# Performance work log

Hardware: AMD Instinct MI355X
Metric: run time of the kernel (lower is better)

The kernel has to match this reference:

```python
import jax, jax.numpy as jnp
import numpy as np

PATCH = 96
STRIDE = PATCH // 2  # 48


def setup_inputs() -> dict:
    key = jax.random.key(0)
    kx = jax.random.fold_in(key, 0)
    x = jax.random.uniform(kx, (8, 4, 1056, 1056), dtype=jnp.float32)
    mu_pristine = jnp.zeros((36,), dtype=jnp.float32)
    cov_pristine = jnp.eye(36, dtype=jnp.float32)
    return {"x": x, "mu_pristine": mu_pristine, "cov_pristine": cov_pristine}


def _extract_patches(x):
    # x: [B, C, H, W] -> overlapping patches [B, C, N, P, P], stride = P//2
    B, C, H, W = x.shape
    nH = (H - PATCH) // STRIDE + 1
    nW = (W - PATCH) // STRIDE + 1
    idx_h = np.arange(nH)[:, None] * STRIDE + np.arange(PATCH)[None, :]  # [nH, P]
    idx_w = np.arange(nW)[:, None] * STRIDE + np.arange(PATCH)[None, :]  # [nW, P]
    p = x[:, :, idx_h, :]            # [B, C, nH, P, W]
    p = p[:, :, :, :, idx_w]         # [B, C, nH, P, nW, P]
    p = p.transpose(0, 1, 2, 4, 3, 5)  # [B, C, nH, nW, P, P]
    return p.reshape(B, C, nH * nW, PATCH, PATCH)


def reference(x, mu_pristine, cov_pristine):
    patches = _extract_patches(x)  # [B, C, N, P, P]
    mu = patches.mean(axis=(-2, -1))                    # [B, C, N]
    var = patches.var(axis=(-2, -1), ddof=1)            # unbiased, matches torch.var
    gx = jnp.diff(patches, axis=-1)                     # [B, C, N, P, P-1]
    gy = jnp.diff(patches, axis=-2)                     # [B, C, N, P-1, P]
    grad_mag = jnp.sqrt((gx * gx).mean(axis=(-2, -1)) + (gy * gy).mean(axis=(-2, -1)))
    # torch concatenates [mu, var, grad_mag] along channel dim per patch, then means over patches
    feats = jnp.concatenate([mu, var, grad_mag], axis=1).mean(axis=-1)  # [B, 3C]
    d = feats.shape[1]
    mu0 = mu_pristine[:d]
    cov_inv = jnp.linalg.inv(cov_pristine[:d, :d])
    diff = feats - mu0[None, :]
    dist = jnp.sqrt(((diff @ cov_inv) * diff).sum(axis=1))  # Mahalanobis distance [B]
    return dist.mean()
```

## Files before the change

kernel.cpp:

```cpp
#include <hip/hip_runtime.h>
#include <math.h>

#define PATCH 96
#define STRIDE 48
#define NH 21
#define NW 21
#define NP (NH * NW)
#define BATCH 8
#define CHAN 4
#define NBC (BATCH * CHAN)
#define IMG_H 1056
#define IMG_W 1056
#define NHB 44
#define NCHUNK 22
#define NSTAT 6
#define NPIX 9216.0f
#define NGRAD 9120.0f
#define SLAB (NHB * NCHUNK * NSTAT)

__global__ __launch_bounds__(320) void band_stats_kernel(
    const float* __restrict__ x, float* __restrict__ pf, int* __restrict__ cnt) {
  __shared__ float acc[NCHUNK * NSTAT];

  const int t = threadIdx.x;
  const int bc = blockIdx.x / NHB;
  const int hb = blockIdx.x - bc * NHB;
  if (blockIdx.x == 0 && t == 0) cnt[0] = 0;

  const bool active = t < 264;
  const int tc = active ? t : 263;
  const int noff = (tc == 263) ? 3 : 4;

  const float* rowbase = x + (size_t)bc * (IMG_H * IMG_W)
                           + (size_t)(hb * 24) * IMG_W
                           + (size_t)(4 * tc);

  float s1 = 0.f, s2 = 0.f, gxi = 0.f, gxb = 0.f, gyi = 0.f, gyb = 0.f;
  const bool bnd_is_gxb = ((tc % 12) == 11);

#define SUMS_GX(A, nxt)                                                  \
  do {                                                                   \
    s1 += (A).x + (A).y + (A).z + (A).w;                                 \
    s2 += (A).x * (A).x + (A).y * (A).y + (A).z * (A).z + (A).w * (A).w; \
    float d1 = (A).y - (A).x, d2 = (A).z - (A).y, d3 = (A).w - (A).z;    \
    float d4 = (nxt) - (A).w;                                            \
    gxi += d1 * d1 + d2 * d2 + d3 * d3;                                  \
    float bd = d4 * d4;                                                  \
    if (bnd_is_gxb) gxb += bd; else gxi += bd;                           \
  } while (0)

  float4 prev;
  {
    const float4 A = *(const float4*)rowbase;
    const float nxt = rowbase[noff];
    SUMS_GX(A, nxt);
    prev = A;
  }
#pragma unroll 4
  for (int r = 1; r < 24; ++r) {
    const float4 A = *(const float4*)(rowbase + (size_t)r * IMG_W);
    const float nxt = rowbase[(size_t)r * IMG_W + noff];
    SUMS_GX(A, nxt);
    const float e0 = A.x - prev.x, e1 = A.y - prev.y,
                e2 = A.z - prev.z, e3 = A.w - prev.w;
    gyi += e0 * e0 + e1 * e1 + e2 * e2 + e3 * e3;
    prev = A;
  }
  if (hb != NHB - 1) {
    const float4 A = *(const float4*)(rowbase + (size_t)24 * IMG_W);
    const float e0 = A.x - prev.x, e1 = A.y - prev.y,
                e2 = A.z - prev.z, e3 = A.w - prev.w;
    gyb = e0 * e0 + e1 * e1 + e2 * e2 + e3 * e3;
  }
#undef SUMS_GX

  for (int i = t; i < NCHUNK * NSTAT; i += 320) acc[i] = 0.f;
  __syncthreads();
  if (active) {
    const int chunk = tc / 12;
    atomicAdd(&acc[chunk * NSTAT + 0], s1);
    atomicAdd(&acc[chunk * NSTAT + 1], s2);
    atomicAdd(&acc[chunk * NSTAT + 2], gxi);
    atomicAdd(&acc[chunk * NSTAT + 3], gxb);
    atomicAdd(&acc[chunk * NSTAT + 4], gyi);
    atomicAdd(&acc[chunk * NSTAT + 5], gyb);
  }
  __syncthreads();
  float* dst = pf + (size_t)(bc * NHB + hb) * (NCHUNK * NSTAT);
  for (int i = t; i < NCHUNK * NSTAT; i += 320) dst[i] = acc[i];
}

__global__ __launch_bounds__(512) void patch_finalize_kernel(
    const float* __restrict__ pf, float* __restrict__ featsG,
    int* __restrict__ cnt, const float* __restrict__ mu0_full,
    const float* __restrict__ cov_full, float* __restrict__ out) {
  __shared__ float S[SLAB];
  __shared__ float wsum[8][3];
  __shared__ double inv_s[12][12];
  __shared__ float fin_s[96 + BATCH];
  __shared__ int ticket_s;

  const int bc = blockIdx.x;
  const int t = threadIdx.x;
  const float* src = pf + (size_t)bc * SLAB;
  for (int i = t; i < SLAB; i += 512) S[i] = src[i];
  __syncthreads();

  float fmu = 0.f, fvar = 0.f, fg = 0.f;
  if (t < NP) {
    const int ph = t / NW, pw = t - ph * NW;
    const int h0 = 2 * ph;
#define AT(h, c, s) S[((h) * NCHUNK + (c)) * NSTAT + (s)]
    float S1 = 0.f, S2 = 0.f, Gx = 0.f, Gy = 0.f;
#pragma unroll
    for (int hh = 0; hh < 4; ++hh) {
      const int h = h0 + hh;
      S1 += AT(h, pw, 0) + AT(h, pw + 1, 0);
      S2 += AT(h, pw, 1) + AT(h, pw + 1, 1);
      Gx += AT(h, pw, 2) + AT(h, pw, 3) + AT(h, pw + 1, 2);
      Gy += AT(h, pw, 4) + AT(h, pw + 1, 4);
    }
#pragma unroll
    for (int hh = 0; hh < 3; ++hh) {
      const int h = h0 + hh;
      Gy += AT(h, pw, 5) + AT(h, pw + 1, 5);
    }
#undef AT
    fmu = S1 / NPIX;
    fvar = (S2 - S1 * S1 / NPIX) / (NPIX - 1.f);
    fg = sqrtf((Gx + Gy) / NGRAD);
  }
#pragma unroll
  for (int off = 32; off > 0; off >>= 1) {
    fmu += __shfl_xor(fmu, off);
    fvar += __shfl_xor(fvar, off);
    fg += __shfl_xor(fg, off);
  }
  const int wave = t >> 6;
  if ((t & 63) == 0) { wsum[wave][0] = fmu; wsum[wave][1] = fvar; wsum[wave][2] = fg; }
  __syncthreads();
  if (t == 0) {
    float m = 0.f, v = 0.f, g = 0.f;
#pragma unroll
    for (int w = 0; w < 8; ++w) { m += wsum[w][0]; v += wsum[w][1]; g += wsum[w][2]; }
    const int b = bc / CHAN, c = bc - b * CHAN;
    featsG[b * 12 + 0 + c] = m / (float)NP;
    featsG[b * 12 + 4 + c] = v / (float)NP;
    featsG[b * 12 + 8 + c] = g / (float)NP;
    __threadfence();
    ticket_s = atomicAdd(cnt, 1);
  }
  __syncthreads();
  if (ticket_s != NBC - 1) return;

  __threadfence();
  if (t < 96)
    fin_s[t] = __hip_atomic_load(&featsG[t], __ATOMIC_RELAXED,
                                 __HIP_MEMORY_SCOPE_AGENT);
  __syncthreads();

  if (t < 64) {
    double M[12];
#pragma unroll
    for (int r = 0; r < 12; ++r) {
      double v = 0.0;
      if (t < 12) v = (double)cov_full[r * 36 + t];
      else if (t < 24) v = (t - 12 == r) ? 1.0 : 0.0;
      M[r] = v;
    }
#pragma unroll
    for (int k = 0; k < 12; ++k) {
      const double piv = __shfl(M[k], k);
      const double ip = 1.0 / piv;
      M[k] *= ip;
#pragma unroll
      for (int r = 0; r < 12; ++r) {
        if (r == k) continue;
        const double f = __shfl(M[r], k);
        M[r] -= f * M[k];
      }
    }
    if (t >= 12 && t < 24) {
      const int j = t - 12;
#pragma unroll
      for (int r = 0; r < 12; ++r) inv_s[r][j] = M[r];
    }
  }
  __syncthreads();

  if (t < BATCH) {
    double acc = 0.0;
    double d[12];
#pragma unroll
    for (int i = 0; i < 12; ++i)
      d[i] = (double)fin_s[t * 12 + i] - (double)mu0_full[i];
#pragma unroll
    for (int i = 0; i < 12; ++i) {
      double row = 0.0;
#pragma unroll
      for (int j = 0; j < 12; ++j) row += inv_s[i][j] * d[j];
      acc += d[i] * row;
    }
    fin_s[96 + t] = (float)sqrt(acc);
  }
  __syncthreads();
  if (t == 0) {
    float m = 0.f;
#pragma unroll
    for (int b = 0; b < BATCH; ++b) m += fin_s[96 + b];
    out[0] = m / (float)BATCH;
  }
}

extern "C" void kernel_launch(void* const* d_in, const int* in_sizes, int n_in,
                              void* d_out, int out_size, void* d_ws, size_t ws_size,
                              hipStream_t stream) {
  const float* x   = (const float*)d_in[0];
  const float* mu0 = (const float*)d_in[1];
  const float* cov = (const float*)d_in[2];
  float* out = (float*)d_out;
  float* pf     = (float*)d_ws;
  float* featsG = pf + (size_t)NBC * SLAB;
  int* cnt      = (int*)(featsG + 96);

  band_stats_kernel<<<NBC * NHB, 320, 0, stream>>>(x, pf, cnt);
  patch_finalize_kernel<<<NBC, 512, 0, stream>>>(pf, featsG, cnt, mu0, cov, out);
}
```

Measured before the change: 227.6 us.

## Double-buffer row bands into LDS with async global_load_lds staging

Each block's band rows are now staged five at a time into a double-buffered LDS tile using the AMD global-to-LDS direct load builtin. The next row group is prefetched while the current one is processed, so each thread's float4 and neighbour reads come from LDS instead of separate global loads. The goal is to overlap memory latency with compute and remove the redundant global read of the neighbour element. The cost is about 42 KB of LDS per block, which limits occupancy, plus extra barriers. It also depends on the compiler inserting the right wait counts before each barrier.

Result: slower. 238.2 us (+4.7%).

```diff
diff --git a/kernel.cpp b/kernel.cpp
--- a/kernel.cpp
+++ b/kernel.cpp
@@ -11,15 +11,25 @@
 #define NBC (BATCH * CHAN)
 #define IMG_H 1056
 #define IMG_W 1056
+#define ROWF 1056
 #define NHB 44
 #define NCHUNK 22
 #define NSTAT 6
 #define NPIX 9216.0f
 #define NGRAD 9120.0f
 #define SLAB (NHB * NCHUNK * NSTAT)
+#define RB 5
+
+typedef __attribute__((address_space(3))) unsigned int lds_uint;
+typedef __attribute__((address_space(1))) const unsigned int glb_uint;
+
+__device__ __forceinline__ void stage16(const float* g, float* l) {
+  __builtin_amdgcn_global_load_lds((glb_uint*)g, (lds_uint*)l, 16, 0, 0);
+}
 
 __global__ __launch_bounds__(320) void band_stats_kernel(
     const float* __restrict__ x, float* __restrict__ pf, int* __restrict__ cnt) {
+  __shared__ float L[2][RB * ROWF];
   __shared__ float acc[NCHUNK * NSTAT];
 
   const int t = threadIdx.x;
@@ -31,12 +41,26 @@
   const int tc = active ? t : 263;
   const int noff = (tc == 263) ? 3 : 4;
 
-  const float* rowbase = x + (size_t)bc * (IMG_H * IMG_W)
-                           + (size_t)(hb * 24) * IMG_W
-                           + (size_t)(4 * tc);
+  const float* base = x + (size_t)bc * (IMG_H * IMG_W);
+  const int row0 = hb * 24;
+  const int wbase = (t >> 6) << 8;
+
+#define STAGE(bt, bufi)                                                   \
+  do {                                                                    \
+    if (active) {                                                         \
+      _Pragma("unroll")                                                   \
+      for (int rr = 0; rr < RB; ++rr) {                                   \
+        int grow = row0 + (bt) * RB + rr;                                 \
+        if (grow > IMG_H - 1) grow = IMG_H - 1;                           \
+        stage16(base + (size_t)grow * ROWF + 4 * tc,                      \
+                &L[bufi][rr * ROWF + wbase]);                             \
+      }                                                                   \
+    }                                                                     \
+  } while (0)
 
   float s1 = 0.f, s2 = 0.f, gxi = 0.f, gxb = 0.f, gyi = 0.f, gyb = 0.f;
   const bool bnd_is_gxb = ((tc % 12) == 11);
+  float4 prev{0.f, 0.f, 0.f, 0.f};
 
 #define SUMS_GX(A, nxt)                                                  \
   do {                                                                   \
@@ -49,30 +73,32 @@
     if (bnd_is_gxb) gxb += bd; else gxi += bd;                           \
   } while (0)
 
-  float4 prev;
-  {
-    const float4 A = *(const float4*)rowbase;
-    const float nxt = rowbase[noff];
-    SUMS_GX(A, nxt);
-    prev = A;
-  }
-#pragma unroll 4
-  for (int r = 1; r < 24; ++r) {
-    const float4 A = *(const float4*)(rowbase + (size_t)r * IMG_W);
-    const float nxt = rowbase[(size_t)r * IMG_W + noff];
-    SUMS_GX(A, nxt);
-    const float e0 = A.x - prev.x, e1 = A.y - prev.y,
-                e2 = A.z - prev.z, e3 = A.w - prev.w;
-    gyi += e0 * e0 + e1 * e1 + e2 * e2 + e3 * e3;
-    prev = A;
-  }
-  if (hb != NHB - 1) {
-    const float4 A = *(const float4*)(rowbase + (size_t)24 * IMG_W);
-    const float e0 = A.x - prev.x, e1 = A.y - prev.y,
-                e2 = A.z - prev.z, e3 = A.w - prev.w;
-    gyb = e0 * e0 + e1 * e1 + e2 * e2 + e3 * e3;
+  STAGE(0, 0);
+  __syncthreads();
+#pragma unroll
+  for (int bt = 0; bt < 5; ++bt) {
+    if (bt < 4) STAGE(bt + 1, (bt + 1) & 1);
+    const float* Lb = &L[bt & 1][0];
+#pragma unroll
+    for (int rr = 0; rr < RB; ++rr) {
+      const int ri = bt * RB + rr;
+      const float4 A = *(const float4*)&Lb[rr * ROWF + 4 * tc];
+      if (ri < 24) {
+        const float nxt = Lb[rr * ROWF + 4 * tc + noff];
+        SUMS_GX(A, nxt);
+      }
+      if (ri > 0) {
+        const float e0 = A.x - prev.x, e1 = A.y - prev.y,
+                    e2 = A.z - prev.z, e3 = A.w - prev.w;
+        const float sq = e0 * e0 + e1 * e1 + e2 * e2 + e3 * e3;
+        if (ri < 24) gyi += sq; else gyb += sq;
+      }
+      prev = A;
+    }
+    __syncthreads();
   }
 #undef SUMS_GX
+#undef STAGE
 
   for (int i = t; i < NCHUNK * NSTAT; i += 320) acc[i] = 0.f;
   __syncthreads();
```

## Stage row loads into LDS asynchronously with a four-row software prefetch pipeline

Applied to the files above, without the earlier changes.

Replaces the per-row direct float4 global loads in the band statistics kernel with `global_load_lds` transfers into a five-slot per-wave LDS ring. Loads are issued four rows ahead and throttled by explicit `s_waitcnt vmcnt` counts, and the loop is fully unrolled. The goal is to keep more memory requests in flight and hide global latency in a kernel whose effective bandwidth is far below peak. It relies on exact hand-counted vmcnt values and on the LDS load builtin's per-lane layout. On the last band the extra boundary row is redirected to a valid row.

New measurement: 240.8 us. +5.8%, slower.

```diff
diff --git a/kernel.cpp b/kernel.cpp
--- a/kernel.cpp
+++ b/kernel.cpp
@@ -11,15 +11,26 @@
 #define NBC (BATCH * CHAN)
 #define IMG_H 1056
 #define IMG_W 1056
+#define ROWF 1056
 #define NHB 44
 #define NCHUNK 22
 #define NSTAT 6
 #define NPIX 9216.0f
 #define NGRAD 9120.0f
 #define SLAB (NHB * NCHUNK * NSTAT)
+#define NR 5
+#define PF 4
+
+typedef __attribute__((address_space(3))) unsigned int lds_uint;
+typedef __attribute__((address_space(1))) const unsigned int glb_uint;
+
+__device__ __forceinline__ void stage16(const float* g, float* l) {
+  __builtin_amdgcn_global_load_lds((glb_uint*)g, (lds_uint*)l, 16, 0, 0);
+}
 
 __global__ __launch_bounds__(320) void band_stats_kernel(
-    const float* __restrict__ x, float* __restrict__ pf, int* __restrict__ cnt) {
+    const float* __restrict__ x, float* __restrict__ pfo, int* __restrict__ cnt) {
+  __shared__ float L[5 * NR * 256];
   __shared__ float acc[NCHUNK * NSTAT];
 
   const int t = threadIdx.x;
@@ -30,49 +41,70 @@
   const bool active = t < 264;
   const int tc = active ? t : 263;
   const int noff = (tc == 263) ? 3 : 4;
-
-  const float* rowbase = x + (size_t)bc * (IMG_H * IMG_W)
-                           + (size_t)(hb * 24) * IMG_W
-                           + (size_t)(4 * tc);
+  const int lane = t & 63;
+  const int wave = t >> 6;
+
+  const float* base = x + (size_t)bc * (IMG_H * IMG_W);
+  const int row0 = hb * 24;
+  float* Lw = &L[wave * (NR * 256)];
 
   float s1 = 0.f, s2 = 0.f, gxi = 0.f, gxb = 0.f, gyi = 0.f, gyb = 0.f;
   const bool bnd_is_gxb = ((tc % 12) == 11);
-
-#define SUMS_GX(A, nxt)                                                  \
+  float4 prev{0.f, 0.f, 0.f, 0.f};
+  float nxt[NR];
+
+#define GROWN(r) (((r) == 24 && hb == NHB - 1) ? (row0 + 23) : (row0 + (r)))
+
+#define ISSUE(r)                                                         \
+  do {                                                                   \
+    const float* g_ = base + (size_t)GROWN(r) * ROWF + 4 * tc;           \
+    stage16(g_, Lw + ((r) % NR) * 256);                                  \
+    nxt[(r) % NR] = g_[noff];                                            \
+  } while (0)
+
+#define SUMS_GX(A, nx)                                                   \
   do {                                                                   \
     s1 += (A).x + (A).y + (A).z + (A).w;                                 \
     s2 += (A).x * (A).x + (A).y * (A).y + (A).z * (A).z + (A).w * (A).w; \
     float d1 = (A).y - (A).x, d2 = (A).z - (A).y, d3 = (A).w - (A).z;    \
-    float d4 = (nxt) - (A).w;                                            \
+    float d4 = (nx) - (A).w;                                             \
     gxi += d1 * d1 + d2 * d2 + d3 * d3;                                  \
     float bd = d4 * d4;                                                  \
     if (bnd_is_gxb) gxb += bd; else gxi += bd;                           \
   } while (0)
 
-  float4 prev;
-  {
-    const float4 A = *(const float4*)rowbase;
-    const float nxt = rowbase[noff];
-    SUMS_GX(A, nxt);
-    prev = A;
-  }
-#pragma unroll 4
-  for (int r = 1; r < 24; ++r) {
-    const float4 A = *(const float4*)(rowbase + (size_t)r * IMG_W);
-    const float nxt = rowbase[(size_t)r * IMG_W + noff];
-    SUMS_GX(A, nxt);
-    const float e0 = A.x - prev.x, e1 = A.y - prev.y,
-                e2 = A.z - prev.z, e3 = A.w - prev.w;
-    gyi += e0 * e0 + e1 * e1 + e2 * e2 + e3 * e3;
-    prev = A;
-  }
-  if (hb != NHB - 1) {
-    const float4 A = *(const float4*)(rowbase + (size_t)24 * IMG_W);
-    const float e0 = A.x - prev.x, e1 = A.y - prev.y,
-                e2 = A.z - prev.z, e3 = A.w - prev.w;
-    gyb = e0 * e0 + e1 * e1 + e2 * e2 + e3 * e3;
-  }
+#define CONSUME(r)                                                       \
+  do {                                                                   \
+    const float4 A = *(const float4*)(Lw + ((r) % NR) * 256 + lane * 4); \
+    if ((r) < 24) SUMS_GX(A, nxt[(r) % NR]);                             \
+    if ((r) > 0) {                                                       \
+      const float e0 = A.x - prev.x, e1 = A.y - prev.y,                  \
+                  e2 = A.z - prev.z, e3 = A.w - prev.w;                  \
+      const float sq = e0 * e0 + e1 * e1 + e2 * e2 + e3 * e3;            \
+      if ((r) < 24) gyi += sq; else gyb += sq;                           \
+    }                                                                    \
+    prev = A;                                                            \
+  } while (0)
+
+#define STEP(r, w)                                                       \
+  do {                                                                   \
+    if ((r) + PF <= 24) ISSUE((r) + PF);                                 \
+    asm volatile("s_waitcnt vmcnt(" #w ")" ::: "memory");                \
+    CONSUME(r);                                                          \
+  } while (0)
+
+  ISSUE(0); ISSUE(1); ISSUE(2); ISSUE(3);
+  STEP(0, 8);  STEP(1, 8);  STEP(2, 8);  STEP(3, 8);  STEP(4, 8);
+  STEP(5, 8);  STEP(6, 8);  STEP(7, 8);  STEP(8, 8);  STEP(9, 8);
+  STEP(10, 8); STEP(11, 8); STEP(12, 8); STEP(13, 8); STEP(14, 8);
+  STEP(15, 8); STEP(16, 8); STEP(17, 8); STEP(18, 8); STEP(19, 8);
+  STEP(20, 8);
+  STEP(21, 6); STEP(22, 4); STEP(23, 2); STEP(24, 0);
+#undef STEP
+#undef CONSUME
 #undef SUMS_GX
+#undef ISSUE
+#undef GROWN
 
   for (int i = t; i < NCHUNK * NSTAT; i += 320) acc[i] = 0.f;
   __syncthreads();
@@ -86,7 +118,7 @@
     atomicAdd(&acc[chunk * NSTAT + 5], gyb);
   }
   __syncthreads();
-  float* dst = pf + (size_t)(bc * NHB + hb) * (NCHUNK * NSTAT);
+  float* dst = pfo + (size_t)(bc * NHB + hb) * (NCHUNK * NSTAT);
   for (int i = t; i < NCHUNK * NSTAT; i += 320) dst[i] = acc[i];
 }
 
```

## Drop per-block LDS atomics; write per-column partials and reduce in finalize

Applied to the files above, without the earlier changes.

The stats kernel no longer pads threads to 320 per band or accumulates into shared memory with atomics. Instead it launches exactly one thread per 4-column strip and writes six per-thread partial sums straight to global memory in a column-major layout. The finalize kernel now performs the 12-wide chunk reduction while loading its shared slab. This removes shared-memory atomics, block syncs and idle threads from the bandwidth-bound stage. In exchange it writes a much larger partial buffer and makes the single-wave-per-image finalize kernel do extra strided global reads.

After: 230.9 us. Within noise of the previous version (+1.4%).

```diff
diff --git a/kernel.cpp b/kernel.cpp
--- a/kernel.cpp
+++ b/kernel.cpp
@@ -11,42 +11,40 @@
 #define NBC (BATCH * CHAN)
 #define IMG_H 1056
 #define IMG_W 1056
+#define ROWF 1056
 #define NHB 44
+#define NQ 264
 #define NCHUNK 22
 #define NSTAT 6
 #define NPIX 9216.0f
 #define NGRAD 9120.0f
-#define SLAB (NHB * NCHUNK * NSTAT)
-
-__global__ __launch_bounds__(320) void band_stats_kernel(
+#define CSLAB (NHB * NCHUNK * NSTAT)
+#define QSLAB (NHB * NSTAT * NQ)
+#define NTHREADS (NBC * NHB * NQ)
+
+__global__ __launch_bounds__(256) void strip_stats_kernel(
     const float* __restrict__ x, float* __restrict__ pf, int* __restrict__ cnt) {
-  __shared__ float acc[NCHUNK * NSTAT];
-
-  const int t = threadIdx.x;
-  const int bc = blockIdx.x / NHB;
-  const int hb = blockIdx.x - bc * NHB;
-  if (blockIdx.x == 0 && t == 0) cnt[0] = 0;
-
-  const bool active = t < 264;
-  const int tc = active ? t : 263;
-  const int noff = (tc == 263) ? 3 : 4;
-
-  const float* rowbase = x + (size_t)bc * (IMG_H * IMG_W)
-                           + (size_t)(hb * 24) * IMG_W
-                           + (size_t)(4 * tc);
+  const int g = blockIdx.x * 256 + threadIdx.x;
+  if (g == 0) cnt[0] = 0;
+
+  const int qcol = g % NQ;
+  const int bh = g / NQ;
+  const int hb = bh % NHB;
+  const int noff = (qcol == NQ - 1) ? 3 : 4;
+
+  const float* rowbase = x + (size_t)(bh / NHB) * (IMG_H * IMG_W)
+                           + (size_t)(hb * 24) * ROWF + 4 * qcol;
 
   float s1 = 0.f, s2 = 0.f, gxi = 0.f, gxb = 0.f, gyi = 0.f, gyb = 0.f;
-  const bool bnd_is_gxb = ((tc % 12) == 11);
-
-#define SUMS_GX(A, nxt)                                                  \
+
+#define SUMS_GX(A, nx)                                                   \
   do {                                                                   \
     s1 += (A).x + (A).y + (A).z + (A).w;                                 \
     s2 += (A).x * (A).x + (A).y * (A).y + (A).z * (A).z + (A).w * (A).w; \
     float d1 = (A).y - (A).x, d2 = (A).z - (A).y, d3 = (A).w - (A).z;    \
-    float d4 = (nxt) - (A).w;                                            \
+    float d4 = (nx) - (A).w;                                             \
     gxi += d1 * d1 + d2 * d2 + d3 * d3;                                  \
-    float bd = d4 * d4;                                                  \
-    if (bnd_is_gxb) gxb += bd; else gxi += bd;                           \
+    gxb += d4 * d4;                                                      \
   } while (0)
 
   float4 prev;
@@ -56,45 +54,39 @@
     SUMS_GX(A, nxt);
     prev = A;
   }
-#pragma unroll 4
+#pragma unroll
   for (int r = 1; r < 24; ++r) {
-    const float4 A = *(const float4*)(rowbase + (size_t)r * IMG_W);
-    const float nxt = rowbase[(size_t)r * IMG_W + noff];
+    const float4 A = *(const float4*)(rowbase + (size_t)r * ROWF);
+    const float nxt = rowbase[(size_t)r * ROWF + noff];
     SUMS_GX(A, nxt);
     const float e0 = A.x - prev.x, e1 = A.y - prev.y,
                 e2 = A.z - prev.z, e3 = A.w - prev.w;
     gyi += e0 * e0 + e1 * e1 + e2 * e2 + e3 * e3;
     prev = A;
   }
-  if (hb != NHB - 1) {
-    const float4 A = *(const float4*)(rowbase + (size_t)24 * IMG_W);
+  {
+    const int r24 = (hb == NHB - 1) ? 23 : 24;
+    const float4 A = *(const float4*)(rowbase + (size_t)r24 * ROWF);
     const float e0 = A.x - prev.x, e1 = A.y - prev.y,
                 e2 = A.z - prev.z, e3 = A.w - prev.w;
     gyb = e0 * e0 + e1 * e1 + e2 * e2 + e3 * e3;
   }
 #undef SUMS_GX
 
-  for (int i = t; i < NCHUNK * NSTAT; i += 320) acc[i] = 0.f;
-  __syncthreads();
-  if (active) {
-    const int chunk = tc / 12;
-    atomicAdd(&acc[chunk * NSTAT + 0], s1);
-    atomicAdd(&acc[chunk * NSTAT + 1], s2);
-    atomicAdd(&acc[chunk * NSTAT + 2], gxi);
-    atomicAdd(&acc[chunk * NSTAT + 3], gxb);
-    atomicAdd(&acc[chunk * NSTAT + 4], gyi);
-    atomicAdd(&acc[chunk * NSTAT + 5], gyb);
-  }
-  __syncthreads();
-  float* dst = pf + (size_t)(bc * NHB + hb) * (NCHUNK * NSTAT);
-  for (int i = t; i < NCHUNK * NSTAT; i += 320) dst[i] = acc[i];
+  float* dst = pf + (size_t)bh * (NSTAT * NQ) + qcol;
+  dst[0 * NQ] = s1;
+  dst[1 * NQ] = s2;
+  dst[2 * NQ] = gxi;
+  dst[3 * NQ] = gxb;
+  dst[4 * NQ] = gyi;
+  dst[5 * NQ] = gyb;
 }
 
 __global__ __launch_bounds__(512) void patch_finalize_kernel(
     const float* __restrict__ pf, float* __restrict__ featsG,
     int* __restrict__ cnt, const float* __restrict__ mu0_full,
     const float* __restrict__ cov_full, float* __restrict__ out) {
-  __shared__ float S[SLAB];
+  __shared__ float S[CSLAB];
   __shared__ float wsum[8][3];
   __shared__ double inv_s[12][12];
   __shared__ float fin_s[96 + BATCH];
@@ -102,8 +94,29 @@
 
   const int bc = blockIdx.x;
   const int t = threadIdx.x;
-  const float* src = pf + (size_t)bc * SLAB;
-  for (int i = t; i < SLAB; i += 512) S[i] = src[i];
+  const float* pb = pf + (size_t)bc * QSLAB;
+
+  for (int i = t; i < CSLAB; i += 512) {
+    const int hb = i / (NCHUNK * NSTAT);
+    const int rem = i - hb * (NCHUNK * NSTAT);
+    const int c = rem / NSTAT;
+    const int s = rem - c * NSTAT;
+    const float* q = pb + (size_t)(hb * NSTAT + s) * NQ + 12 * c;
+    float v;
+    if (s == 3) {
+      v = q[11];
+    } else {
+      v = 0.f;
+#pragma unroll
+      for (int k = 0; k < 12; ++k) v += q[k];
+      if (s == 2) {
+        const float* qb = q + NQ;
+#pragma unroll
+        for (int k = 0; k < 11; ++k) v += qb[k];
+      }
+    }
+    S[i] = v;
+  }
   __syncthreads();
 
   float fmu = 0.f, fvar = 0.f, fg = 0.f;
@@ -220,9 +233,9 @@
   const float* cov = (const float*)d_in[2];
   float* out = (float*)d_out;
   float* pf     = (float*)d_ws;
-  float* featsG = pf + (size_t)NBC * SLAB;
+  float* featsG = pf + (size_t)NBC * QSLAB;
   int* cnt      = (int*)(featsG + 96);
 
-  band_stats_kernel<<<NBC * NHB, 320, 0, stream>>>(x, pf, cnt);
+  strip_stats_kernel<<<NTHREADS / 256, 256, 0, stream>>>(x, pf, cnt);
   patch_finalize_kernel<<<NBC, 512, 0, stream>>>(pf, featsG, cnt, mu0, cov, out);
 }
```
